# Performance work log

Measured on AMD Instinct MI355X. Metric: run time of the kernel, lower is better.

Reference implementation:

```python
import jax, jax.numpy as jnp
import numpy as np

N = 50000      # nodes
E = 800000     # edges
IN = 128       # in_ch
OUT = 32       # out_ch
H = 4          # heads
ED = 16        # edge_dim
SLOPE = 0.2    # LeakyReLU negative slope (GATv2 default and outer activation)


def setup_inputs() -> dict:
    key = jax.random.key(0)
    ks = jax.random.split(key, 10)
    s_in = 1.0 / np.sqrt(IN)
    s_ed = 1.0 / np.sqrt(ED)
    s_out = 1.0 / np.sqrt(OUT)
    return {
        "x": jax.random.normal(ks[0], (N, IN), jnp.float32),
        "edge_index": jax.random.randint(ks[1], (2, E), 0, N, dtype=jnp.int32),
        "edges_attr": jax.random.normal(ks[2], (E, ED), jnp.float32),
        "W_l": jax.random.normal(ks[3], (IN, H * OUT), jnp.float32) * s_in,
        "b_l": jnp.zeros((H * OUT,), jnp.float32),
        "W_r": jax.random.normal(ks[4], (IN, H * OUT), jnp.float32) * s_in,
        "b_r": jnp.zeros((H * OUT,), jnp.float32),
        "W_e": jax.random.normal(ks[5], (ED, H * OUT), jnp.float32) * s_ed,
        "att": jax.random.normal(ks[6], (H, OUT), jnp.float32) * s_out,
        "bias": jnp.zeros((OUT,), jnp.float32),
    }


def reference(x, edge_index, edges_attr, W_l, b_l, W_r, b_r, W_e, att, bias):
    src, tgt = edge_index[0], edge_index[1]

    # add_self_loops with fill_value='mean': self-loop attr = scatter-mean of
    # incoming edge attrs per target node (0 for isolated nodes, as in PyG).
    deg = jax.ops.segment_sum(jnp.ones((E,), x.dtype), tgt, num_segments=N)
    attr_sum = jax.ops.segment_sum(edges_attr, tgt, num_segments=N)
    loop_attr = attr_sum / jnp.maximum(deg, 1.0)[:, None]
    node_ids = jnp.arange(N, dtype=src.dtype)
    src_f = jnp.concatenate([src, node_ids])   # [E+N]
    tgt_f = jnp.concatenate([tgt, node_ids])   # [E+N]
    attr_f = jnp.concatenate([edges_attr, loop_attr], axis=0)  # [E+N, ED]

    x_l = (x @ W_l + b_l).reshape(N, H, OUT)   # source transform
    x_r = (x @ W_r + b_r).reshape(N, H, OUT)   # target transform
    e = (attr_f @ W_e).reshape(-1, H, OUT)     # edge transform

    # GATv2 score: att . leaky_relu(x_l[j] + x_r[i] + e_ij)
    m = x_l[src_f] + x_r[tgt_f] + e                          # [E+N, H, OUT]
    scores = jnp.einsum('ehc,hc->eh', jax.nn.leaky_relu(m, SLOPE), att)

    # scatter-softmax over edges grouped by target node (every segment has a
    # self-loop, so segment_max is well-defined)
    smax = jax.ops.segment_max(scores, tgt_f, num_segments=N)
    ex = jnp.exp(scores - smax[tgt_f])
    denom = jax.ops.segment_sum(ex, tgt_f, num_segments=N)
    alpha = ex / denom[tgt_f]                                # [E+N, H]

    # weighted aggregation of source messages x_l[j]
    msg = alpha[:, :, None] * x_l[src_f]                     # [E+N, H, OUT]
    out = jax.ops.segment_sum(msg, tgt_f, num_segments=N)   # [N, H, OUT]

    out = out.mean(axis=1) + bias                            # concat=False -> head mean
    return jax.nn.leaky_relu(out, SLOPE)                     # outer LeakyReLU(0.2)
```

## Files before the change

### kernel.cpp

```cpp
#include <hip/hip_runtime.h>
#include <hip/hip_fp16.h>
#include <math.h>

#define NN 50000
#define NE 800000
#define SLOPE 0.2f
#define NB 49
#define GEMMB 782
#define EDGEB 3125

typedef __attribute__((ext_vector_type(8))) short bf16x8;
typedef __attribute__((ext_vector_type(4))) float f32x4;
typedef _Float16 half2v __attribute__((ext_vector_type(2)));

#if __has_builtin(__builtin_amdgcn_fdot2)
#define FDOT2(A, B, C) __builtin_amdgcn_fdot2((A), (B), (C), false)
#else
#define FDOT2(A, B, C) \
  fmaf((float)(A).x, (float)(B).x, fmaf((float)(A).y, (float)(B).y, (C)))
#endif

static __device__ __forceinline__ void split_bf16(float v, unsigned short& h,
                                                  unsigned short& l) {
  unsigned u = __float_as_uint(v);
  h = (unsigned short)(u >> 16);
  float hf = __uint_as_float(((unsigned)h) << 16);
  float r = v - hf;
  l = (unsigned short)(__float_as_uint(r) >> 16);
}


__device__ __forceinline__ void gemm_body(int bx, const float* __restrict__ x,
                                          const float* __restrict__ W,
                                          const float* __restrict__ bptr,
                                          __half* __restrict__ optr,
                                          unsigned short* xh_s, unsigned short* xl_s,
                                          unsigned short* wh_s, unsigned short* wl_s) {
  int tid = threadIdx.x;
  int w = tid >> 6;
  int l = tid & 63;
  int n0 = bx * 64;

  f32x4 acc[8];
#pragma unroll
  for (int i = 0; i < 8; ++i) acc[i] = (f32x4){0.f, 0.f, 0.f, 0.f};

  for (int kb = 0; kb < 128; kb += 32) {
    {
      int row = tid >> 2;
      int kc = (tid & 3) * 8;
      int gn = n0 + row;
      float4 v0 = make_float4(0.f, 0.f, 0.f, 0.f);
      float4 v1 = make_float4(0.f, 0.f, 0.f, 0.f);
      if (gn < NN) {
        v0 = *(const float4*)(x + (size_t)gn * 128 + kb + kc);
        v1 = *(const float4*)(x + (size_t)gn * 128 + kb + kc + 4);
      }
      unsigned short h[8], lo[8];
      split_bf16(v0.x, h[0], lo[0]); split_bf16(v0.y, h[1], lo[1]);
      split_bf16(v0.z, h[2], lo[2]); split_bf16(v0.w, h[3], lo[3]);
      split_bf16(v1.x, h[4], lo[4]); split_bf16(v1.y, h[5], lo[5]);
      split_bf16(v1.z, h[6], lo[6]); split_bf16(v1.w, h[7], lo[7]);
      bf16x8 hv, lv;
#pragma unroll
      for (int i = 0; i < 8; ++i) { hv[i] = (short)h[i]; lv[i] = (short)lo[i]; }
      *(bf16x8*)&xh_s[row * 40 + kc] = hv;
      *(bf16x8*)&xl_s[row * 40 + kc] = lv;
    }
    {
      int col = tid & 127;
      int kk0 = (tid >> 7) * 16;
      unsigned short h[16], lo[16];
#pragma unroll
      for (int j = 0; j < 16; ++j)
        split_bf16(W[(size_t)(kb + kk0 + j) * 128 + col], h[j], lo[j]);
      bf16x8 hv0, hv1, lv0, lv1;
#pragma unroll
      for (int i = 0; i < 8; ++i) {
        hv0[i] = (short)h[i]; hv1[i] = (short)h[8 + i];
        lv0[i] = (short)lo[i]; lv1[i] = (short)lo[8 + i];
      }
      *(bf16x8*)&wh_s[col * 40 + kk0] = hv0;
      *(bf16x8*)&wh_s[col * 40 + kk0 + 8] = hv1;
      *(bf16x8*)&wl_s[col * 40 + kk0] = lv0;
      *(bf16x8*)&wl_s[col * 40 + kk0 + 8] = lv1;
    }
    __syncthreads();

    int r16 = 16 * w + (l & 15);
    int ko = (l >> 4) * 8;
    bf16x8 ah = *(bf16x8*)&xh_s[r16 * 40 + ko];
    bf16x8 al = *(bf16x8*)&xl_s[r16 * 40 + ko];
#pragma unroll
    for (int ct = 0; ct < 8; ++ct) {
      int cbase = (ct * 16 + (l & 15)) * 40 + ko;
      bf16x8 bh = *(bf16x8*)&wh_s[cbase];
      bf16x8 bl = *(bf16x8*)&wl_s[cbase];
      acc[ct] = __builtin_amdgcn_mfma_f32_16x16x32_bf16(ah, bh, acc[ct], 0, 0, 0);
      acc[ct] = __builtin_amdgcn_mfma_f32_16x16x32_bf16(al, bh, acc[ct], 0, 0, 0);
      acc[ct] = __builtin_amdgcn_mfma_f32_16x16x32_bf16(ah, bl, acc[ct], 0, 0, 0);
    }
    __syncthreads();
  }

  int colb = l & 15;
  int rq = (l >> 4) * 4;
#pragma unroll
  for (int ct = 0; ct < 8; ++ct) {
    float bvv = bptr[ct * 16 + colb];
#pragma unroll
    for (int r = 0; r < 4; ++r) {
      int gn = n0 + 16 * w + rq + r;
      if (gn < NN)
        optr[(size_t)gn * 128 + ct * 16 + colb] = __float2half(acc[ct][r] + bvv);
    }
  }
}


__launch_bounds__(256)
__global__ void fusedA_kernel(const float* __restrict__ x,
                              const float* __restrict__ W_l, const float* __restrict__ b_l,
                              __half* __restrict__ x_l,
                              const int* __restrict__ tgt, int* __restrict__ deg,
                              int* __restrict__ rank) {
  __shared__ unsigned short xh_s[64 * 40], xl_s[64 * 40];
  __shared__ unsigned short wh_s[128 * 40], wl_s[128 * 40];
  if (blockIdx.x < GEMMB) {
    gemm_body(blockIdx.x, x, W_l, b_l, x_l, xh_s, xl_s, wh_s, wl_s);
  } else {
    int e = (blockIdx.x - GEMMB) * 256 + threadIdx.x;
    if (e < NE) rank[e] = atomicAdd(&deg[tgt[e]], 1);
  }
}


__launch_bounds__(256)
__global__ void fusedB_kernel(const float* __restrict__ x,
                              const float* __restrict__ W_r, const float* __restrict__ b_r,
                              __half* __restrict__ x_r,
                              const int* __restrict__ src, const int* __restrict__ tgt,
                              const int* __restrict__ rank,
                              const int* __restrict__ rowptr,
                              const float4* __restrict__ eattr4,
                              int* __restrict__ csr_src,
                              unsigned short* __restrict__ eattr_h) {
  __shared__ unsigned short xh_s[64 * 40], xl_s[64 * 40];
  __shared__ unsigned short wh_s[128 * 40], wl_s[128 * 40];
  if (blockIdx.x < GEMMB) {
    gemm_body(blockIdx.x, x, W_r, b_r, x_r, xh_s, xl_s, wh_s, wl_s);
  } else {
    int e = (blockIdx.x - GEMMB) * 256 + threadIdx.x;
    if (e < NE) {
      int t = tgt[e];
      int r = rank[e];
      float4 a0 = eattr4[(size_t)e * 4 + 0];
      float4 a1 = eattr4[(size_t)e * 4 + 1];
      float4 a2 = eattr4[(size_t)e * 4 + 2];
      float4 a3 = eattr4[(size_t)e * 4 + 3];
      __half2 q0 = __float22half2_rn(make_float2(a0.x, a0.y));
      __half2 q1 = __float22half2_rn(make_float2(a0.z, a0.w));
      __half2 q2 = __float22half2_rn(make_float2(a1.x, a1.y));
      __half2 q3 = __float22half2_rn(make_float2(a1.z, a1.w));
      __half2 q4 = __float22half2_rn(make_float2(a2.x, a2.y));
      __half2 q5 = __float22half2_rn(make_float2(a2.z, a2.w));
      __half2 q6 = __float22half2_rn(make_float2(a3.x, a3.y));
      __half2 q7 = __float22half2_rn(make_float2(a3.z, a3.w));
      uint4 u0, u1;
      u0.x = __builtin_bit_cast(unsigned, q0); u0.y = __builtin_bit_cast(unsigned, q1);
      u0.z = __builtin_bit_cast(unsigned, q2); u0.w = __builtin_bit_cast(unsigned, q3);
      u1.x = __builtin_bit_cast(unsigned, q4); u1.y = __builtin_bit_cast(unsigned, q5);
      u1.z = __builtin_bit_cast(unsigned, q6); u1.w = __builtin_bit_cast(unsigned, q7);
      int pos = rowptr[t] + r;
      csr_src[pos] = src[e];
      unsigned short* row = eattr_h + (size_t)pos * 16;
      *(uint4*)row = u0;
      *(uint4*)(row + 8) = u1;
    }
  }
}


__global__ void partial_kernel(const int* __restrict__ deg, int* __restrict__ psum) {
  int b = blockIdx.x;
  int base = b * 1024 + threadIdx.x * 4;
  int s = 0;
  if (base + 3 < NN) {
    int4 v = *(const int4*)(deg + base);
    s = v.x + v.y + v.z + v.w;
  } else {
#pragma unroll
    for (int i = 0; i < 4; ++i)
      if (base + i < NN) s += deg[base + i];
  }
  s += __shfl_xor(s, 1);
  s += __shfl_xor(s, 2);
  s += __shfl_xor(s, 4);
  s += __shfl_xor(s, 8);
  s += __shfl_xor(s, 16);
  s += __shfl_xor(s, 32);
  __shared__ int wsum[4];
  if ((threadIdx.x & 63) == 0) wsum[threadIdx.x >> 6] = s;
  __syncthreads();
  if (threadIdx.x == 0) psum[b] = wsum[0] + wsum[1] + wsum[2] + wsum[3];
}

__global__ void final_kernel(const int* __restrict__ deg, const int* __restrict__ psum,
                             int* __restrict__ rowptr) {
  __shared__ int offs_s;
  __shared__ int wtot[4];
  int b = blockIdx.x;
  int t = threadIdx.x;
  if (t < 64) {
    int lane = t;
    int mine = (lane < NB) ? psum[lane] : 0;
    int v = mine;
#pragma unroll
    for (int off = 1; off < 64; off <<= 1) {
      int u = __shfl_up(v, off);
      if (lane >= off) v += u;
    }
    if (lane == b) offs_s = v - mine;
    if (b == 0 && lane == 63) rowptr[NN] = v;
  }
  __syncthreads();

  int base = b * 1024 + t * 4;
  int d0 = 0, d1 = 0, d2 = 0, d3 = 0;
  if (base + 3 < NN) {
    int4 v = *(const int4*)(deg + base);
    d0 = v.x; d1 = v.y; d2 = v.z; d3 = v.w;
  } else {
    if (base < NN) d0 = deg[base];
    if (base + 1 < NN) d1 = deg[base + 1];
    if (base + 2 < NN) d2 = deg[base + 2];
  }
  int s = d0 + d1 + d2 + d3;
  int lane = t & 63, w = t >> 6;
  int v = s;
#pragma unroll
  for (int off = 1; off < 64; off <<= 1) {
    int u = __shfl_up(v, off);
    if (lane >= off) v += u;
  }
  if (lane == 63) wtot[w] = v;
  __syncthreads();
  int woff = 0;
#pragma unroll
  for (int i = 0; i < 4; ++i)
    if (i < w) woff += wtot[i];
  int run = offs_s + woff + (v - s);
  if (base < NN)     { rowptr[base] = run;     run += d0; }
  if (base + 1 < NN) { rowptr[base + 1] = run; run += d1; }
  if (base + 2 < NN) { rowptr[base + 2] = run; run += d2; }
  if (base + 3 < NN) { rowptr[base + 3] = run; }
}


#define EDGE_PROC_H(AU, XL)                                            \
  {                                                                    \
    float e0 = 0.f, e1 = 0.f;                                          \
    _Pragma("unroll")                                                  \
    for (int jj = 0; jj < 8; ++jj) {                                   \
      half2v ha = __builtin_bit_cast(half2v, AU[jj]);                  \
      e0 = FDOT2(ha, wekA[jj], e0);                                    \
      e1 = FDOT2(ha, wekB[jj], e1);                                    \
    }                                                                  \
    es0 += e0; es1 += e1;                                              \
    float m0 = (XL.x + xr.x) + e0;                                     \
    float m1 = (XL.y + xr.y) + e1;                                     \
    float lm0 = fmaf(SLOPE, fminf(m0, 0.f), fmaxf(m0, 0.f));           \
    float lm1 = fmaf(SLOPE, fminf(m1, 0.f), fmaxf(m1, 0.f));           \
    float part = fmaf(attv.y, lm1, attv.x * lm0);                      \
    part += __shfl_xor(part, 1);                                       \
    part += __shfl_xor(part, 2);                                       \
    part += __shfl_xor(part, 4);                                       \
    part += __shfl_xor(part, 8);                                       \
    float p = __expf(part);                                            \
    lh += p;                                                           \
    acc0 = fmaf(p, XL.x, acc0);                                        \
    acc1 = fmaf(p, XL.y, acc1);                                        \
  }

__launch_bounds__(256)
__global__ void gat_kernel(const __half* __restrict__ x_l, const __half* __restrict__ x_r,
                           const int* __restrict__ rowptr, const int* __restrict__ csr_src,
                           const unsigned short* __restrict__ eattr_h,
                           const float* __restrict__ W_e,
                           const float* __restrict__ att, const float* __restrict__ bias,
                           float* __restrict__ out) {
  int wid = threadIdx.x >> 6;
  int lane = threadIdx.x & 63;
  int tbase = (blockIdx.x * 4 + wid) * 4;

  half2v wekA[8], wekB[8];
#pragma unroll
  for (int j = 0; j < 8; ++j) {
    float2 w0 = *(const float2*)(W_e + (2 * j) * 128 + 2 * lane);
    float2 w1 = *(const float2*)(W_e + (2 * j + 1) * 128 + 2 * lane);
    wekA[j].x = (_Float16)w0.x; wekA[j].y = (_Float16)w1.x;
    wekB[j].x = (_Float16)w0.y; wekB[j].y = (_Float16)w1.y;
  }
  float2 attv = *(const float2*)(att + 2 * lane);
  float bv = bias[(2 * lane) & 31];
  float bv1 = bias[((2 * lane) & 31) + 1];

  for (int tt = 0; tt < 4; ++tt) {
    int t = tbase + tt;
    float2 xr = __half22float2(*(const __half2*)(x_r + (size_t)t * 128 + 2 * lane));
    int start = __builtin_amdgcn_readfirstlane(rowptr[t]);
    int end = __builtin_amdgcn_readfirstlane(rowptr[t + 1]);

    float lh = 0.f, acc0 = 0.f, acc1 = 0.f, es0 = 0.f, es1 = 0.f;

    int j = start;
    for (; j + 4 <= end; j += 4) {
      int s0 = __builtin_amdgcn_readfirstlane(csr_src[j]);
      int s1 = __builtin_amdgcn_readfirstlane(csr_src[j + 1]);
      int s2 = __builtin_amdgcn_readfirstlane(csr_src[j + 2]);
      int s3 = __builtin_amdgcn_readfirstlane(csr_src[j + 3]);
      float2 xl0 = __half22float2(*(const __half2*)(x_l + (size_t)s0 * 128 + 2 * lane));
      float2 xl1 = __half22float2(*(const __half2*)(x_l + (size_t)s1 * 128 + 2 * lane));
      float2 xl2 = __half22float2(*(const __half2*)(x_l + (size_t)s2 * 128 + 2 * lane));
      float2 xl3 = __half22float2(*(const __half2*)(x_l + (size_t)s3 * 128 + 2 * lane));
      const unsigned* apg = (const unsigned*)eattr_h + (size_t)j * 8;
      unsigned A0[8], A1[8], A2[8], A3[8];
#pragma unroll
      for (int k = 0; k < 8; ++k) A0[k] = apg[k];
#pragma unroll
      for (int k = 0; k < 8; ++k) A1[k] = apg[8 + k];
#pragma unroll
      for (int k = 0; k < 8; ++k) A2[k] = apg[16 + k];
#pragma unroll
      for (int k = 0; k < 8; ++k) A3[k] = apg[24 + k];
      EDGE_PROC_H(A0, xl0)
      EDGE_PROC_H(A1, xl1)
      EDGE_PROC_H(A2, xl2)
      EDGE_PROC_H(A3, xl3)
    }
    if (j + 2 <= end) {
      int s0 = __builtin_amdgcn_readfirstlane(csr_src[j]);
      int s1 = __builtin_amdgcn_readfirstlane(csr_src[j + 1]);
      float2 xl0 = __half22float2(*(const __half2*)(x_l + (size_t)s0 * 128 + 2 * lane));
      float2 xl1 = __half22float2(*(const __half2*)(x_l + (size_t)s1 * 128 + 2 * lane));
      const unsigned* apg = (const unsigned*)eattr_h + (size_t)j * 8;
      unsigned A0[8], A1[8];
#pragma unroll
      for (int k = 0; k < 8; ++k) A0[k] = apg[k];
#pragma unroll
      for (int k = 0; k < 8; ++k) A1[k] = apg[8 + k];
      EDGE_PROC_H(A0, xl0)
      EDGE_PROC_H(A1, xl1)
      j += 2;
    }
    if (j < end) {
      int srcn = __builtin_amdgcn_readfirstlane(csr_src[j]);
      float2 xlC = __half22float2(*(const __half2*)(x_l + (size_t)srcn * 128 + 2 * lane));
      const unsigned* apg = (const unsigned*)eattr_h + (size_t)j * 8;
      unsigned A0[8];
#pragma unroll
      for (int k = 0; k < 8; ++k) A0[k] = apg[k];
      EDGE_PROC_H(A0, xlC)
    }

    {
      float rdeg = 1.0f / fmaxf((float)(end - start), 1.0f);
      float e0 = es0 * rdeg, e1 = es1 * rdeg;
      float2 xl = __half22float2(*(const __half2*)(x_l + (size_t)t * 128 + 2 * lane));
      float m0 = (xl.x + xr.x) + e0;
      float m1 = (xl.y + xr.y) + e1;
      float lm0 = fmaf(SLOPE, fminf(m0, 0.f), fmaxf(m0, 0.f));
      float lm1 = fmaf(SLOPE, fminf(m1, 0.f), fmaxf(m1, 0.f));
      float part = fmaf(attv.y, lm1, attv.x * lm0);
      part += __shfl_xor(part, 1);
      part += __shfl_xor(part, 2);
      part += __shfl_xor(part, 4);
      part += __shfl_xor(part, 8);
      float p = __expf(part);
      lh += p;
      acc0 = fmaf(p, xl.x, acc0);
      acc1 = fmaf(p, xl.y, acc1);
    }

    float inv = 1.0f / lh;
    float v0 = acc0 * inv, v1 = acc1 * inv;
    v0 += __shfl_xor(v0, 16);
    v0 += __shfl_xor(v0, 32);
    v1 += __shfl_xor(v1, 16);
    v1 += __shfl_xor(v1, 32);
    if (lane < 16) {
      float o0 = fmaf(v0, 0.25f, bv);
      float o1 = fmaf(v1, 0.25f, bv1);
      o0 = fmaf(SLOPE, fminf(o0, 0.f), fmaxf(o0, 0.f));
      o1 = fmaf(SLOPE, fminf(o1, 0.f), fmaxf(o1, 0.f));
      *(float2*)(out + (size_t)t * 32 + 2 * lane) = make_float2(o0, o1);
    }
  }
}


extern "C" void kernel_launch(void* const* d_in, const int* in_sizes, int n_in,
                              void* d_out, int out_size, void* d_ws, size_t ws_size,
                              hipStream_t stream) {
  const float* x = (const float*)d_in[0];
  const int* ei = (const int*)d_in[1];
  const float* eattr = (const float*)d_in[2];
  const float* W_l = (const float*)d_in[3];
  const float* b_l = (const float*)d_in[4];
  const float* W_r = (const float*)d_in[5];
  const float* b_r = (const float*)d_in[6];
  const float* W_e = (const float*)d_in[7];
  const float* att = (const float*)d_in[8];
  const float* bias = (const float*)d_in[9];
  float* out = (float*)d_out;

  char* ws = (char*)d_ws;
  int* csr_src = (int*)ws;
  unsigned short* eattr_h = (unsigned short*)(ws + 3200000);
  __half* x_l = (__half*)(ws + 28800000);
  __half* x_r = (__half*)(ws + 41600000);
  int* deg = (int*)(ws + 54400000);
  int* rowptr = (int*)(ws + 54600000);
  int* rank = (int*)(ws + 54800016);
  int* psum = (int*)(ws + 58000016);

  hipMemsetAsync(deg, 0, NN * sizeof(int), stream);
  fusedA_kernel<<<GEMMB + EDGEB, 256, 0, stream>>>(x, W_l, b_l, x_l, ei + NE, deg, rank);
  partial_kernel<<<NB, 256, 0, stream>>>(deg, psum);
  final_kernel<<<NB, 256, 0, stream>>>(deg, psum, rowptr);
  fusedB_kernel<<<GEMMB + EDGEB, 256, 0, stream>>>(
      x, W_r, b_r, x_r, ei, ei + NE, rank, rowptr, (const float4*)eattr,
      csr_src, eattr_h);
  gat_kernel<<<NN / 16, 256, 0, stream>>>(x_l, x_r, rowptr, csr_src, eattr_h, W_e, att, bias, out);
}
```

Measured before the change: 282.3 us.

## Privatize degree counters per XCD to cut cross-die atomic contention

Splits the single degree-count array into 8 copies indexed by blockIdx&7, which on MI355X maps blocks round-robin to XCDs, so the atomics stay within one die's L2. The prefix-sum kernels now sum the 8 copies and emit per-bucket absolute offsets, which the scatter kernel uses together with a bucket-tagged rank. This costs a larger memset, 8x the reads in the scan kernels and an extra offsets array.

```diff
diff --git a/kernel.cpp b/kernel.cpp
--- a/kernel.cpp
+++ b/kernel.cpp
@@ -122,7 +122,7 @@
 __global__ void fusedA_kernel(const float* __restrict__ x,
                               const float* __restrict__ W_l, const float* __restrict__ b_l,
                               __half* __restrict__ x_l,
-                              const int* __restrict__ tgt, int* __restrict__ deg,
+                              const int* __restrict__ tgt, int* __restrict__ deg8,
                               int* __restrict__ rank) {
   __shared__ unsigned short xh_s[64 * 40], xl_s[64 * 40];
   __shared__ unsigned short wh_s[128 * 40], wl_s[128 * 40];
@@ -130,7 +130,11 @@
     gemm_body(blockIdx.x, x, W_l, b_l, x_l, xh_s, xl_s, wh_s, wl_s);
   } else {
     int e = (blockIdx.x - GEMMB) * 256 + threadIdx.x;
-    if (e < NE) rank[e] = atomicAdd(&deg[tgt[e]], 1);
+    if (e < NE) {
+      int bkt = blockIdx.x & 7;
+      int r = atomicAdd(&deg8[bkt * NN + tgt[e]], 1);
+      rank[e] = (bkt << 24) | r;
+    }
   }
 }
 
@@ -141,7 +145,7 @@
                               __half* __restrict__ x_r,
                               const int* __restrict__ src, const int* __restrict__ tgt,
                               const int* __restrict__ rank,
-                              const int* __restrict__ rowptr,
+                              const int* __restrict__ xoffabs,
                               const float4* __restrict__ eattr4,
                               int* __restrict__ csr_src,
                               unsigned short* __restrict__ eattr_h) {
@@ -153,7 +157,9 @@
     int e = (blockIdx.x - GEMMB) * 256 + threadIdx.x;
     if (e < NE) {
       int t = tgt[e];
-      int r = rank[e];
+      int rr = rank[e];
+      int bkt = rr >> 24;
+      int r = rr & 0xFFFFFF;
       float4 a0 = eattr4[(size_t)e * 4 + 0];
       float4 a1 = eattr4[(size_t)e * 4 + 1];
       float4 a2 = eattr4[(size_t)e * 4 + 2];
@@ -171,7 +177,7 @@
       u0.z = __builtin_bit_cast(unsigned, q2); u0.w = __builtin_bit_cast(unsigned, q3);
       u1.x = __builtin_bit_cast(unsigned, q4); u1.y = __builtin_bit_cast(unsigned, q5);
       u1.z = __builtin_bit_cast(unsigned, q6); u1.w = __builtin_bit_cast(unsigned, q7);
-      int pos = rowptr[t] + r;
+      int pos = xoffabs[bkt * NN + t] + r;
       csr_src[pos] = src[e];
       unsigned short* row = eattr_h + (size_t)pos * 16;
       *(uint4*)row = u0;
@@ -181,17 +187,22 @@
 }
 
 
-__global__ void partial_kernel(const int* __restrict__ deg, int* __restrict__ psum) {
+__global__ void partial_kernel(const int* __restrict__ deg8, int* __restrict__ psum) {
   int b = blockIdx.x;
   int base = b * 1024 + threadIdx.x * 4;
   int s = 0;
   if (base + 3 < NN) {
-    int4 v = *(const int4*)(deg + base);
-    s = v.x + v.y + v.z + v.w;
+#pragma unroll
+    for (int xcd = 0; xcd < 8; ++xcd) {
+      int4 v = *(const int4*)(deg8 + (size_t)xcd * NN + base);
+      s += v.x + v.y + v.z + v.w;
+    }
   } else {
 #pragma unroll
     for (int i = 0; i < 4; ++i)
-      if (base + i < NN) s += deg[base + i];
+      if (base + i < NN)
+#pragma unroll
+        for (int xcd = 0; xcd < 8; ++xcd) s += deg8[(size_t)xcd * NN + base + i];
   }
   s += __shfl_xor(s, 1);
   s += __shfl_xor(s, 2);
@@ -205,8 +216,8 @@
   if (threadIdx.x == 0) psum[b] = wsum[0] + wsum[1] + wsum[2] + wsum[3];
 }
 
-__global__ void final_kernel(const int* __restrict__ deg, const int* __restrict__ psum,
-                             int* __restrict__ rowptr) {
+__global__ void final_kernel(const int* __restrict__ deg8, const int* __restrict__ psum,
+                             int* __restrict__ rowptr, int* __restrict__ xoffabs) {
   __shared__ int offs_s;
   __shared__ int wtot[4];
   int b = blockIdx.x;
@@ -226,16 +237,26 @@
   __syncthreads();
 
   int base = b * 1024 + t * 4;
-  int d0 = 0, d1 = 0, d2 = 0, d3 = 0;
-  if (base + 3 < NN) {
-    int4 v = *(const int4*)(deg + base);
-    d0 = v.x; d1 = v.y; d2 = v.z; d3 = v.w;
-  } else {
-    if (base < NN) d0 = deg[base];
-    if (base + 1 < NN) d1 = deg[base + 1];
-    if (base + 2 < NN) d2 = deg[base + 2];
-  }
-  int s = d0 + d1 + d2 + d3;
+  int c[8][4];
+#pragma unroll
+  for (int xcd = 0; xcd < 8; ++xcd) {
+    if (base + 3 < NN) {
+      int4 v = *(const int4*)(deg8 + (size_t)xcd * NN + base);
+      c[xcd][0] = v.x; c[xcd][1] = v.y; c[xcd][2] = v.z; c[xcd][3] = v.w;
+    } else {
+#pragma unroll
+      for (int i = 0; i < 4; ++i)
+        c[xcd][i] = (base + i < NN) ? deg8[(size_t)xcd * NN + base + i] : 0;
+    }
+  }
+  int d[4];
+#pragma unroll
+  for (int i = 0; i < 4; ++i) {
+    d[i] = 0;
+#pragma unroll
+    for (int xcd = 0; xcd < 8; ++xcd) d[i] += c[xcd][i];
+  }
+  int s = d[0] + d[1] + d[2] + d[3];
   int lane = t & 63, w = t >> 6;
   int v = s;
 #pragma unroll
@@ -250,10 +271,19 @@
   for (int i = 0; i < 4; ++i)
     if (i < w) woff += wtot[i];
   int run = offs_s + woff + (v - s);
-  if (base < NN)     { rowptr[base] = run;     run += d0; }
-  if (base + 1 < NN) { rowptr[base + 1] = run; run += d1; }
-  if (base + 2 < NN) { rowptr[base + 2] = run; run += d2; }
-  if (base + 3 < NN) { rowptr[base + 3] = run; }
+#pragma unroll
+  for (int i = 0; i < 4; ++i) {
+    if (base + i < NN) {
+      rowptr[base + i] = run;
+      int pref = run;
+#pragma unroll
+      for (int xcd = 0; xcd < 8; ++xcd) {
+        xoffabs[(size_t)xcd * NN + base + i] = pref;
+        pref += c[xcd][i];
+      }
+      run += d[i];
+    }
+  }
 }
 
 
@@ -419,17 +449,18 @@
   unsigned short* eattr_h = (unsigned short*)(ws + 3200000);
   __half* x_l = (__half*)(ws + 28800000);
   __half* x_r = (__half*)(ws + 41600000);
-  int* deg = (int*)(ws + 54400000);
-  int* rowptr = (int*)(ws + 54600000);
-  int* rank = (int*)(ws + 54800016);
-  int* psum = (int*)(ws + 58000016);
-
-  hipMemsetAsync(deg, 0, NN * sizeof(int), stream);
-  fusedA_kernel<<<GEMMB + EDGEB, 256, 0, stream>>>(x, W_l, b_l, x_l, ei + NE, deg, rank);
-  partial_kernel<<<NB, 256, 0, stream>>>(deg, psum);
-  final_kernel<<<NB, 256, 0, stream>>>(deg, psum, rowptr);
+  int* deg8 = (int*)(ws + 54400000);
+  int* rowptr = (int*)(ws + 56000000);
+  int* rank = (int*)(ws + 56200016);
+  int* xoffabs = (int*)(ws + 59400016);
+  int* psum = (int*)(ws + 61000016);
+
+  hipMemsetAsync(deg8, 0, 8 * NN * sizeof(int), stream);
+  fusedA_kernel<<<GEMMB + EDGEB, 256, 0, stream>>>(x, W_l, b_l, x_l, ei + NE, deg8, rank);
+  partial_kernel<<<NB, 256, 0, stream>>>(deg8, psum);
+  final_kernel<<<NB, 256, 0, stream>>>(deg8, psum, rowptr, xoffabs);
   fusedB_kernel<<<GEMMB + EDGEB, 256, 0, stream>>>(
-      x, W_r, b_r, x_r, ei, ei + NE, rank, rowptr, (const float4*)eattr,
+      x, W_r, b_r, x_r, ei, ei + NE, rank, xoffabs, (const float4*)eattr,
       csr_src, eattr_h);
   gat_kernel<<<NN / 16, 256, 0, stream>>>(x_l, x_r, rowptr, csr_src, eattr_h, W_e, att, bias, out);
 }
```

Result: no change. 280.5 us (-0.6%).
